# Performance work log

Measured on AMD Instinct MI355X. Metric: run time of the kernel, lower is better.

Reference implementation:

```python
import jax, jax.numpy as jnp
import numpy as np

B, T, D, H, L, O = 256, 256, 64, 512, 2, 10


def _uniform(key, shape, scale):
    return jax.random.uniform(key, shape, jnp.float32, -scale, scale)


def setup_inputs() -> dict:
    key = jax.random.key(0)
    ks = jax.random.split(key, 16)
    s = 1.0 / np.sqrt(H)  # PyTorch default init bound for RNN and Linear(H, .)
    inp = {
        "x": jax.random.normal(ks[0], (B, T, D), jnp.float32),
        # layer 0: input D -> H
        "w_ih0": _uniform(ks[1], (H, D), s),
        "w_hh0": _uniform(ks[2], (H, H), s),
        "b_ih0": _uniform(ks[3], (H,), s),
        "b_hh0": _uniform(ks[4], (H,), s),
        # layer 1: H -> H
        "w_ih1": _uniform(ks[5], (H, H), s),
        "w_hh1": _uniform(ks[6], (H, H), s),
        "b_ih1": _uniform(ks[7], (H,), s),
        "b_hh1": _uniform(ks[8], (H,), s),
        # head: fc1 (H->8), fc2 (8->O)
        "fc1_w": _uniform(ks[9], (8, H), s),
        "fc1_b": _uniform(ks[10], (8,), s),
        "fc2_w": _uniform(ks[11], (O, 8), 1.0 / np.sqrt(8)),
        "fc2_b": _uniform(ks[12], (O,), 1.0 / np.sqrt(8)),
    }
    return inp


def _rnn_relu_layer(seq, w_ih, w_hh, b_ih, b_hh):
    # seq: [T, B, Din] -> out: [T, B, H]
    # Precompute input projection for all timesteps (one big GEMM).
    x_proj = jnp.einsum('tbd,hd->tbh', seq, w_ih) + b_ih + b_hh

    def step(h, xp):
        h = jax.nn.relu(xp + h @ w_hh.T)
        return h, h

    h0 = jnp.zeros((seq.shape[1], w_hh.shape[0]), seq.dtype)
    _, out = jax.lax.scan(step, h0, x_proj)
    return out


def reference(x, w_ih0, w_hh0, b_ih0, b_hh0, w_ih1, w_hh1, b_ih1, b_hh1,
              fc1_w, fc1_b, fc2_w, fc2_b):
    seq = jnp.transpose(x, (1, 0, 2))  # [T, B, D]
    seq = _rnn_relu_layer(seq, w_ih0, w_hh0, b_ih0, b_hh0)
    seq = _rnn_relu_layer(seq, w_ih1, w_hh1, b_ih1, b_hh1)
    last = seq[-1]  # [B, H]
    h = jax.nn.relu(last @ fc1_w.T + fc1_b)
    return h @ fc2_w.T + fc2_b  # [B, O]
```

## Files before the change

### kernel.cpp

```cpp
#include <hip/hip_runtime.h>

using bf16x8 = __attribute__((ext_vector_type(8))) short;
using f32x4  = __attribute__((ext_vector_type(4))) float;
typedef unsigned short u16;
typedef unsigned int   u32;
typedef unsigned long long u64;

#define MAX_SPIN 1000000


__device__ __forceinline__ float bf2f(u16 u){ union{u32 i;float f;}v; v.i=((u32)u)<<16; return v.f; }
__device__ __forceinline__ u16 f2bf(float f){ union{float f;u32 i;}v; v.f=f; u32 x=v.i; return (u16)((x+0x7FFFu+((x>>16)&1u))>>16); }
__device__ __forceinline__ u32 packhl(float v){ u16 hi=f2bf(v); u16 lo=f2bf(v-bf2f(hi)); return ((u32)hi<<16)|(u32)lo; }
__device__ __forceinline__ bf16x8 load8f(const float* p){
  float4 a=*(const float4*)p; float4 b=*(const float4*)(p+4);
  bf16x8 r; r[0]=(short)f2bf(a.x); r[1]=(short)f2bf(a.y); r[2]=(short)f2bf(a.z); r[3]=(short)f2bf(a.w);
  r[4]=(short)f2bf(b.x); r[5]=(short)f2bf(b.y); r[6]=(short)f2bf(b.z); r[7]=(short)f2bf(b.w); return r;
}
__device__ __forceinline__ int  ldf(const int* p){ return __hip_atomic_load(p, __ATOMIC_RELAXED, __HIP_MEMORY_SCOPE_AGENT); }
__device__ __forceinline__ u64 ld64c(const u32* p){ return __hip_atomic_load((const u64*)p, __ATOMIC_RELAXED, __HIP_MEMORY_SCOPE_AGENT); }
__device__ __forceinline__ u32 ld32c(const u32* p){ return __hip_atomic_load(p, __ATOMIC_RELAXED, __HIP_MEMORY_SCOPE_AGENT); }
__device__ __forceinline__ void st32c(u32* p, u32 v){ __hip_atomic_store(p, v, __ATOMIC_RELAXED, __HIP_MEMORY_SCOPE_AGENT); }

__global__ void init_kernel(u32* p){
  p[(blockIdx.x<<9) + threadIdx.x] = 0u;
}

__global__ void __launch_bounds__(512, 2)
rnn_kernel(const float* __restrict__ x,
           const float* __restrict__ w_ih0, const float* __restrict__ w_hh0,
           const float* __restrict__ b_ih0, const float* __restrict__ b_hh0,
           const float* __restrict__ w_ih1, const float* __restrict__ w_hh1,
           const float* __restrict__ b_ih1, const float* __restrict__ b_hh1,
           const float* __restrict__ fc1_w, const float* __restrict__ fc1_b,
           const float* __restrict__ fc2_w, const float* __restrict__ fc2_b,
           float* __restrict__ out,
           u32* __restrict__ ring0, u32* __restrict__ ring1,
           int* __restrict__ fl0, int* __restrict__ fl1)
{
  const int tid  = threadIdx.x;
  const int wg   = blockIdx.x;
  const int lane = tid & 63;
  const int ww   = tid >> 6;
  const int role = wg >> 4;
  const int bt   = wg & 15;
  const int b0   = bt << 4;
  const int lrow = lane & 15;
  const int lk8  = (lane >> 4) << 3;
  const int sw   = (lrow & 7) << 4;

  __shared__ char smA[32768];
  __shared__ char smB[32768];

  if (role < 2) {
    const int nbase = role << 8;
    bf16x8 wH0[16], wH1[16], wX0[2], wX1[2];
    float bias0, bias1;
    {
      const int n0c = nbase + (ww << 5) + lrow;
      const int n1c = n0c + 16;
#pragma unroll
      for (int ks = 0; ks < 16; ++ks) {
        wH0[ks] = load8f(w_hh0 + n0c*512 + (ks<<5) + lk8);
        wH1[ks] = load8f(w_hh0 + n1c*512 + (ks<<5) + lk8);
      }
      wX0[0] = load8f(w_ih0 + n0c*64 + lk8);  wX0[1] = load8f(w_ih0 + n0c*64 + 32 + lk8);
      wX1[0] = load8f(w_ih0 + n1c*64 + lk8);  wX1[1] = load8f(w_ih0 + n1c*64 + 32 + lk8);
      bias0 = b_ih0[n0c] + b_hh0[n0c];
      bias1 = b_ih0[n1c] + b_hh0[n1c];
    }

    for (int s = 0; s < 256; ++s) {
      {
        int idx = tid << 1, r = idx >> 6, c = idx & 63;
        const float* xp = x + ((size_t)((b0 + r) << 8) + s) * 64 + c;
        float2 xv = *(const float2*)xp;
        u32 e0 = packhl(xv.x), e1 = packhl(xv.y);
        u32 hiw = (e0 >> 16) | (e1 & 0xFFFF0000u);
        u32 low = (e0 & 0xFFFFu) | (e1 << 16);
        int xo = (r << 7) + (((c << 1)) ^ ((r & 7) << 4));
        *(u32*)(smB + xo) = hiw;  *(u32*)(smB + 16384 + xo) = low;
      }
      __syncthreads();
      f32x4 acc0 = {0.f,0.f,0.f,0.f}, acc1 = {0.f,0.f,0.f,0.f};
#pragma unroll
      for (int ks = 0; ks < 2; ++ks) {
        int off = (lrow << 7) + (((ks << 6) + (lk8 << 1)) ^ sw);
        bf16x8 ahi = *(const bf16x8*)(smB + off);
        bf16x8 alo = *(const bf16x8*)(smB + 16384 + off);
        acc0 = __builtin_amdgcn_mfma_f32_16x16x32_bf16(ahi, wX0[ks], acc0, 0,0,0);
        acc0 = __builtin_amdgcn_mfma_f32_16x16x32_bf16(alo, wX0[ks], acc0, 0,0,0);
        acc1 = __builtin_amdgcn_mfma_f32_16x16x32_bf16(ahi, wX1[ks], acc1, 0,0,0);
        acc1 = __builtin_amdgcn_mfma_f32_16x16x32_bf16(alo, wX1[ks], acc1, 0,0,0);
      }
      if (ww == 0) {
        const int* f0p = fl0 + ((s - 1) << 4) + bt;
        const int* f1p = fl1 + ((s - 4) << 4) + bt;
        int it = 0;
        for (;;) {
          bool ok = true;
          if (s >= 1 && ldf(f0p) < 2) ok = false;
          if (ok && s >= 4 && ldf(f1p) < 4) ok = false;
          if (ok || ++it > MAX_SPIN) break;
        }
      }
      __syncthreads();
      if (s >= 1) {
        const u32* rs = ring0 + (((s - 1) & 3) << 17) + (b0 << 9);
#pragma unroll
        for (int k = 0; k < 8; ++k) {
          int q = tid + (k << 9);
          int r = q >> 8, c = q & 255;
          u64 v = ld64c(rs + (r << 9) + (c << 1));
          u32 e0 = (u32)v, e1 = (u32)(v >> 32);
          u32 hiw = (e0 >> 16) | (e1 & 0xFFFF0000u);
          u32 low = (e0 & 0xFFFFu) | (e1 << 16);
          int o = (r << 10) + ((c << 2) ^ ((r & 7) << 4));
          *(u32*)(smA + o) = hiw;  *(u32*)(smA + 16384 + o) = low;
        }
        __syncthreads();
#pragma unroll
        for (int ks = 0; ks < 16; ++ks) {
          int off = (lrow << 10) + (((ks << 6) + (lk8 << 1)) ^ sw);
          bf16x8 ahi = *(const bf16x8*)(smA + off);
          bf16x8 alo = *(const bf16x8*)(smA + 16384 + off);
          acc0 = __builtin_amdgcn_mfma_f32_16x16x32_bf16(ahi, wH0[ks], acc0, 0,0,0);
          acc0 = __builtin_amdgcn_mfma_f32_16x16x32_bf16(alo, wH0[ks], acc0, 0,0,0);
          acc1 = __builtin_amdgcn_mfma_f32_16x16x32_bf16(ahi, wH1[ks], acc1, 0,0,0);
          acc1 = __builtin_amdgcn_mfma_f32_16x16x32_bf16(alo, wH1[ks], acc1, 0,0,0);
        }
      }
      {
        u32* wsl = ring0 + ((s & 3) << 17) + (b0 << 9);
        int rr0 = (lane >> 4) << 2;
        int nc0 = nbase + (ww << 5) + lrow, nc1 = nc0 + 16;
#pragma unroll
        for (int r = 0; r < 4; ++r) {
          float v0 = acc0[r] + bias0; v0 = v0 > 0.f ? v0 : 0.f;
          float v1 = acc1[r] + bias1; v1 = v1 > 0.f ? v1 : 0.f;
          st32c(wsl + ((rr0 + r) << 9) + nc0, packhl(v0));
          st32c(wsl + ((rr0 + r) << 9) + nc1, packhl(v1));
        }
      }
      asm volatile("s_waitcnt vmcnt(0)" ::: "memory");
      __syncthreads();
      if (tid == 0)
        __hip_atomic_fetch_add(fl0 + (s << 4) + bt, 1, __ATOMIC_RELAXED, __HIP_MEMORY_SCOPE_AGENT);
    }
  } else {
    const int nbase = (role - 2) << 7;
    bf16x8 wI[16], wHH[16];
    float bias;
    {
      const int n = nbase + (ww << 4) + lrow;
#pragma unroll
      for (int ks = 0; ks < 16; ++ks) {
        wI[ks]  = load8f(w_ih1 + n*512 + (ks<<5) + lk8);
        wHH[ks] = load8f(w_hh1 + n*512 + (ks<<5) + lk8);
      }
      bias = b_ih1[n] + b_hh1[n];
    }

    for (int t = 0; t < 256; ++t) {
      if (ww == 0) {
        const int* f0p = fl0 + (t << 4) + bt;
        const int* f1p = fl1 + ((t - 1) << 4) + bt;
        int it = 0;
        for (;;) {
          bool ok = (ldf(f0p) >= 2);
          if (ok && t >= 1 && ldf(f1p) < 4) ok = false;
          if (ok || ++it > MAX_SPIN) break;
        }
      }
      __syncthreads();
      {
        const u32* ra = ring0 + ((t & 3) << 17) + (b0 << 9);
        const u32* rb = ring1 + (((t - 1) & 3) << 17) + (b0 << 9);
#pragma unroll
        for (int k = 0; k < 8; ++k) {
          int q = tid + (k << 9);
          int r = q >> 8, c = q & 255;
          int o = (r << 10) + ((c << 2) ^ ((r & 7) << 4));
          u64 v = ld64c(ra + (r << 9) + (c << 1));
          u32 e0 = (u32)v, e1 = (u32)(v >> 32);
          *(u32*)(smA + o)         = (e0 >> 16) | (e1 & 0xFFFF0000u);
          *(u32*)(smA + 16384 + o) = (e0 & 0xFFFFu) | (e1 << 16);
          if (t >= 1) {
            u64 w = ld64c(rb + (r << 9) + (c << 1));
            u32 f0v = (u32)w, f1v = (u32)(w >> 32);
            *(u32*)(smB + o)         = (f0v >> 16) | (f1v & 0xFFFF0000u);
            *(u32*)(smB + 16384 + o) = (f0v & 0xFFFFu) | (f1v << 16);
          }
        }
      }
      __syncthreads();
      f32x4 acc = {0.f,0.f,0.f,0.f};
      if (t == 0) {
#pragma unroll
        for (int ks = 0; ks < 16; ++ks) {
          int off = (lrow << 10) + (((ks << 6) + (lk8 << 1)) ^ sw);
          bf16x8 ahi = *(const bf16x8*)(smA + off);
          bf16x8 alo = *(const bf16x8*)(smA + 16384 + off);
          acc = __builtin_amdgcn_mfma_f32_16x16x32_bf16(ahi, wI[ks], acc, 0,0,0);
          acc = __builtin_amdgcn_mfma_f32_16x16x32_bf16(alo, wI[ks], acc, 0,0,0);
        }
      } else {
#pragma unroll
        for (int ks = 0; ks < 16; ++ks) {
          int off = (lrow << 10) + (((ks << 6) + (lk8 << 1)) ^ sw);
          bf16x8 ahi = *(const bf16x8*)(smA + off);
          bf16x8 alo = *(const bf16x8*)(smA + 16384 + off);
          bf16x8 bhi = *(const bf16x8*)(smB + off);
          bf16x8 blo = *(const bf16x8*)(smB + 16384 + off);
          acc = __builtin_amdgcn_mfma_f32_16x16x32_bf16(ahi, wI[ks],  acc, 0,0,0);
          acc = __builtin_amdgcn_mfma_f32_16x16x32_bf16(alo, wI[ks],  acc, 0,0,0);
          acc = __builtin_amdgcn_mfma_f32_16x16x32_bf16(bhi, wHH[ks], acc, 0,0,0);
          acc = __builtin_amdgcn_mfma_f32_16x16x32_bf16(blo, wHH[ks], acc, 0,0,0);
        }
      }
      {
        u32* wsl = ring1 + ((t & 3) << 17) + (b0 << 9);
        int rr0 = (lane >> 4) << 2;
        int nc = nbase + (ww << 4) + lrow;
#pragma unroll
        for (int r = 0; r < 4; ++r) {
          float v = acc[r] + bias; v = v > 0.f ? v : 0.f;
          st32c(wsl + ((rr0 + r) << 9) + nc, packhl(v));
        }
      }
      asm volatile("s_waitcnt vmcnt(0)" ::: "memory");
      __syncthreads();
      if (tid == 0)
        __hip_atomic_fetch_add(fl1 + (t << 4) + bt, 1, __ATOMIC_RELAXED, __HIP_MEMORY_SCOPE_AGENT);
    }

    if (role == 2) {
      if (ww == 0) {
        const int* fp = fl1 + (255 << 4) + bt;
        int it = 0;
        while (ldf(fp) < 4) { if (++it > MAX_SPIN) break; }
      }
      __syncthreads();
      float* smF = (float*)smA;
      if (tid < 128) {
        int b = b0 + (tid >> 3), j = tid & 7;
        const u32* hp = ring1 + (3 << 17) + (b << 9);
        const float* wr = fc1_w + (j << 9);
        float accv = fc1_b[j];
        for (int k = 0; k < 512; k += 2) {
          u64 v = ld64c(hp + k);
          u32 e0 = (u32)v, e1 = (u32)(v >> 32);
          float h0v = bf2f((u16)(e0 >> 16)) + bf2f((u16)(e0 & 0xFFFFu));
          float h1v = bf2f((u16)(e1 >> 16)) + bf2f((u16)(e1 & 0xFFFFu));
          accv += h0v * wr[k] + h1v * wr[k + 1];
        }
        smF[tid] = accv > 0.f ? accv : 0.f;
      }
      __syncthreads();
      if (tid < 160) {
        int bb = tid / 10, o = tid - bb * 10;
        float accv = fc2_b[o];
        const float* w = fc2_w + (o << 3);
#pragma unroll
        for (int j = 0; j < 8; ++j) accv += smF[(bb << 3) + j] * w[j];
        out[(b0 + bb) * 10 + o] = accv;
      }
    }
  }
}

extern "C" void kernel_launch(void* const* d_in, const int* in_sizes, int n_in,
                              void* d_out, int out_size, void* d_ws, size_t ws_size,
                              hipStream_t stream) {
  const float* x     = (const float*)d_in[0];
  const float* w_ih0 = (const float*)d_in[1];
  const float* w_hh0 = (const float*)d_in[2];
  const float* b_ih0 = (const float*)d_in[3];
  const float* b_hh0 = (const float*)d_in[4];
  const float* w_ih1 = (const float*)d_in[5];
  const float* w_hh1 = (const float*)d_in[6];
  const float* b_ih1 = (const float*)d_in[7];
  const float* b_hh1 = (const float*)d_in[8];
  const float* fc1_w = (const float*)d_in[9];
  const float* fc1_b = (const float*)d_in[10];
  const float* fc2_w = (const float*)d_in[11];
  const float* fc2_b = (const float*)d_in[12];
  float* out = (float*)d_out;

  char* ws = (char*)d_ws;
  u32* ring0 = (u32*)(ws);
  u32* ring1 = (u32*)(ws + (2 << 20));
  int* fl0   = (int*)(ws + (4 << 20));
  int* fl1   = (int*)(ws + (4 << 20) + 16384);

  init_kernel<<<dim3(16), dim3(512), 0, stream>>>((u32*)(ws + (4 << 20)));
  rnn_kernel<<<dim3(96), dim3(512), 0, stream>>>(
      x, w_ih0, w_hh0, b_ih0, b_hh0, w_ih1, w_hh1, b_ih1, b_hh1,
      fc1_w, fc1_b, fc2_w, fc2_b, out, ring0, ring1, fl0, fl1);
}
```

Measured before the change: 1.667 ms.

## Restructure RNN pipeline into per-batch-tile role workgroups with keeps-own-state recurrence

Reorganizes the persistent kernel into five roles per batch tile: a layer-0 recurrent WG and a layer-1 recurrent WG that each hold the full hidden state in LDS, two WGs computing the layer-1 input projection, and one WG computing the layer-0 input projection ahead of time. Each recurrent WG keeps W_hh partly in registers and partly in LDS, so the serial recurrence no longer needs a cross-workgroup exchange of the hidden state through global memory every step. Only precomputed projections go through global rings, with simple monotonic per-tile flags and s_sleep backoff. The cost is a large 160KB LDS footprint per WG and a longer dependency chain across more workgroups, which adds deadlock risk if not all 80 WGs are co-resident.

```diff
diff --git a/kernel.cpp b/kernel.cpp
--- a/kernel.cpp
+++ b/kernel.cpp
@@ -6,25 +6,30 @@
 typedef unsigned int   u32;
 typedef unsigned long long u64;
 
-#define MAX_SPIN 1000000
+#define MAX_SPIN 2000000
 
 
 __device__ __forceinline__ float bf2f(u16 u){ union{u32 i;float f;}v; v.i=((u32)u)<<16; return v.f; }
 __device__ __forceinline__ u16 f2bf(float f){ union{float f;u32 i;}v; v.f=f; u32 x=v.i; return (u16)((x+0x7FFFu+((x>>16)&1u))>>16); }
-__device__ __forceinline__ u32 packhl(float v){ u16 hi=f2bf(v); u16 lo=f2bf(v-bf2f(hi)); return ((u32)hi<<16)|(u32)lo; }
 __device__ __forceinline__ bf16x8 load8f(const float* p){
   float4 a=*(const float4*)p; float4 b=*(const float4*)(p+4);
   bf16x8 r; r[0]=(short)f2bf(a.x); r[1]=(short)f2bf(a.y); r[2]=(short)f2bf(a.z); r[3]=(short)f2bf(a.w);
   r[4]=(short)f2bf(b.x); r[5]=(short)f2bf(b.y); r[6]=(short)f2bf(b.z); r[7]=(short)f2bf(b.w); return r;
 }
-__device__ __forceinline__ int  ldf(const int* p){ return __hip_atomic_load(p, __ATOMIC_RELAXED, __HIP_MEMORY_SCOPE_AGENT); }
-__device__ __forceinline__ u64 ld64c(const u32* p){ return __hip_atomic_load((const u64*)p, __ATOMIC_RELAXED, __HIP_MEMORY_SCOPE_AGENT); }
-__device__ __forceinline__ u32 ld32c(const u32* p){ return __hip_atomic_load(p, __ATOMIC_RELAXED, __HIP_MEMORY_SCOPE_AGENT); }
+__device__ __forceinline__ int  ldf(int* p){ return __hip_atomic_load(p, __ATOMIC_RELAXED, __HIP_MEMORY_SCOPE_AGENT); }
+__device__ __forceinline__ void stf(int* p, int v){ __hip_atomic_store(p, v, __ATOMIC_RELAXED, __HIP_MEMORY_SCOPE_AGENT); }
+__device__ __forceinline__ u64  ld64c(const u32* p){ return __hip_atomic_load((const u64*)p, __ATOMIC_RELAXED, __HIP_MEMORY_SCOPE_AGENT); }
+__device__ __forceinline__ u32  ld32c(const u32* p){ return __hip_atomic_load(p, __ATOMIC_RELAXED, __HIP_MEMORY_SCOPE_AGENT); }
 __device__ __forceinline__ void st32c(u32* p, u32 v){ __hip_atomic_store(p, v, __ATOMIC_RELAXED, __HIP_MEMORY_SCOPE_AGENT); }
-
-__global__ void init_kernel(u32* p){
-  p[(blockIdx.x<<9) + threadIdx.x] = 0u;
+__device__ __forceinline__ int waitge(int* p, int tgt){
+  int v = ldf(p); int it = 0;
+  while (v < tgt && ++it < MAX_SPIN){ __builtin_amdgcn_s_sleep(1); v = ldf(p); }
+  return v;
 }
+
+__global__ void init_kernel(u32* p){ p[(blockIdx.x<<9) + threadIdx.x] = 0u; }
+
+#define HFRAG(base, ks) (*(const bf16x8*)((base) + (lrow<<10) + ((((ks)<<6)+(lk8<<1)) ^ sw)))
 
 __global__ void __launch_bounds__(512, 2)
 rnn_kernel(const float* __restrict__ x,
@@ -35,8 +40,8 @@
            const float* __restrict__ fc1_w, const float* __restrict__ fc1_b,
            const float* __restrict__ fc2_w, const float* __restrict__ fc2_b,
            float* __restrict__ out,
-           u32* __restrict__ ring0, u32* __restrict__ ring1,
-           int* __restrict__ fl0, int* __restrict__ fl1)
+           u32* __restrict__ ring0, u32* __restrict__ ringz0, u32* __restrict__ ringz1,
+           int* __restrict__ flags)
 {
   const int tid  = threadIdx.x;
   const int wg   = blockIdx.x;
@@ -48,223 +53,281 @@
   const int lrow = lane & 15;
   const int lk8  = (lane >> 4) << 3;
   const int sw   = (lrow & 7) << 4;
-
-  __shared__ char smA[32768];
-  __shared__ char smB[32768];
-
-  if (role < 2) {
-    const int nbase = role << 8;
-    bf16x8 wH0[16], wH1[16], wX0[2], wX1[2];
-    float bias0, bias1;
-    {
-      const int n0c = nbase + (ww << 5) + lrow;
-      const int n1c = n0c + 16;
-#pragma unroll
-      for (int ks = 0; ks < 16; ++ks) {
-        wH0[ks] = load8f(w_hh0 + n0c*512 + (ks<<5) + lk8);
-        wH1[ks] = load8f(w_hh0 + n1c*512 + (ks<<5) + lk8);
-      }
-      wX0[0] = load8f(w_ih0 + n0c*64 + lk8);  wX0[1] = load8f(w_ih0 + n0c*64 + 32 + lk8);
-      wX1[0] = load8f(w_ih0 + n1c*64 + lk8);  wX1[1] = load8f(w_ih0 + n1c*64 + 32 + lk8);
-      bias0 = b_ih0[n0c] + b_hh0[n0c];
-      bias1 = b_ih0[n1c] + b_hh0[n1c];
+  const int rb   = (lane >> 4) << 2;
+
+  extern __shared__ char dummy_unused[];
+  __shared__ char sm[163840];
+  char* smWb  = sm;
+  char* smHhi = sm + 131072;
+  char* smHlo = sm + 147456;
+
+  int* flA  = flags + ((bt<<3) + 0)*16;
+  int* flB0 = flags + ((bt<<3) + 1)*16;
+  int* flB1 = flags + ((bt<<3) + 2)*16;
+  int* flC  = flags + ((bt<<3) + 3)*16;
+  int* flD  = flags + ((bt<<3) + 4)*16;
+
+  if (role == 0 || role == 1) {
+    const float* Wp = (role == 0) ? w_hh0 : w_hh1;
+    const int n0 = ww << 6;
+    bf16x8 wv[48];
+#pragma unroll
+    for (int tt = 0; tt < 4; ++tt) {
+      int n = n0 + (tt<<4) + lrow;
+#pragma unroll
+      for (int ks = 0; ks < 12; ++ks)
+        wv[tt*12+ks] = load8f(Wp + n*512 + (ks<<5) + lk8);
+    }
+#pragma unroll 1
+    for (int it = 0; it < 16; ++it) {
+      int cid = (it<<9) + tid;
+      int ss = cid >> 11, wc = cid & 2047;
+      int n = wc >> 2, k0 = (wc & 3) << 3;
+      bf16x8 v = load8f(Wp + n*512 + 384 + (ss<<5) + k0);
+      *(bf16x8*)(smWb + (ss<<15) + (n<<6) + ((k0<<1) ^ ((n&3)<<4))) = v;
+    }
+    __syncthreads();
+
+    const int wl0 = ((lane>>4)<<4) ^ ((lrow&3)<<4);
+    int wlb[4];
+#pragma unroll
+    for (int tt = 0; tt < 4; ++tt) wlb[tt] = ((n0 + (tt<<4) + lrow)<<6) + wl0;
+
+    float zpf[16];
+    int f0v = 0, f1v = 0;
+    u32* zring = (role == 0) ? ringz0 : ringz1;
+    const u32* zbase = zring + bt*32768;
+    if (role == 0) { f0v = waitge(flD, 1); }
+    else           { f0v = waitge(flB0, 1); f1v = waitge(flB1, 1); }
+#pragma unroll
+    for (int tt = 0; tt < 4; ++tt) {
+      int nc = n0 + (tt<<4) + lrow;
+#pragma unroll
+      for (int r = 0; r < 4; ++r)
+        zpf[tt*4+r] = __uint_as_float(ld32c(zbase + ((rb+r)<<9) + nc));
     }
 
     for (int s = 0; s < 256; ++s) {
-      {
-        int idx = tid << 1, r = idx >> 6, c = idx & 63;
-        const float* xp = x + ((size_t)((b0 + r) << 8) + s) * 64 + c;
-        float2 xv = *(const float2*)xp;
-        u32 e0 = packhl(xv.x), e1 = packhl(xv.y);
-        u32 hiw = (e0 >> 16) | (e1 & 0xFFFF0000u);
-        u32 low = (e0 & 0xFFFFu) | (e1 << 16);
-        int xo = (r << 7) + (((c << 1)) ^ ((r & 7) << 4));
-        *(u32*)(smB + xo) = hiw;  *(u32*)(smB + 16384 + xo) = low;
-      }
-      __syncthreads();
-      f32x4 acc0 = {0.f,0.f,0.f,0.f}, acc1 = {0.f,0.f,0.f,0.f};
-#pragma unroll
-      for (int ks = 0; ks < 2; ++ks) {
-        int off = (lrow << 7) + (((ks << 6) + (lk8 << 1)) ^ sw);
-        bf16x8 ahi = *(const bf16x8*)(smB + off);
-        bf16x8 alo = *(const bf16x8*)(smB + 16384 + off);
-        acc0 = __builtin_amdgcn_mfma_f32_16x16x32_bf16(ahi, wX0[ks], acc0, 0,0,0);
-        acc0 = __builtin_amdgcn_mfma_f32_16x16x32_bf16(alo, wX0[ks], acc0, 0,0,0);
-        acc1 = __builtin_amdgcn_mfma_f32_16x16x32_bf16(ahi, wX1[ks], acc1, 0,0,0);
-        acc1 = __builtin_amdgcn_mfma_f32_16x16x32_bf16(alo, wX1[ks], acc1, 0,0,0);
-      }
-      if (ww == 0) {
-        const int* f0p = fl0 + ((s - 1) << 4) + bt;
-        const int* f1p = fl1 + ((s - 4) << 4) + bt;
-        int it = 0;
-        for (;;) {
-          bool ok = true;
-          if (s >= 1 && ldf(f0p) < 2) ok = false;
-          if (ok && s >= 4 && ldf(f1p) < 4) ok = false;
-          if (ok || ++it > MAX_SPIN) break;
-        }
-      }
-      __syncthreads();
-      if (s >= 1) {
-        const u32* rs = ring0 + (((s - 1) & 3) << 17) + (b0 << 9);
-#pragma unroll
-        for (int k = 0; k < 8; ++k) {
-          int q = tid + (k << 9);
-          int r = q >> 8, c = q & 255;
-          u64 v = ld64c(rs + (r << 9) + (c << 1));
-          u32 e0 = (u32)v, e1 = (u32)(v >> 32);
-          u32 hiw = (e0 >> 16) | (e1 & 0xFFFF0000u);
-          u32 low = (e0 & 0xFFFFu) | (e1 << 16);
-          int o = (r << 10) + ((c << 2) ^ ((r & 7) << 4));
-          *(u32*)(smA + o) = hiw;  *(u32*)(smA + 16384 + o) = low;
-        }
-        __syncthreads();
+      f32x4 acc[4] = {{0,0,0,0},{0,0,0,0},{0,0,0,0},{0,0,0,0}};
+      if (s > 0) {
 #pragma unroll
         for (int ks = 0; ks < 16; ++ks) {
-          int off = (lrow << 10) + (((ks << 6) + (lk8 << 1)) ^ sw);
-          bf16x8 ahi = *(const bf16x8*)(smA + off);
-          bf16x8 alo = *(const bf16x8*)(smA + 16384 + off);
-          acc0 = __builtin_amdgcn_mfma_f32_16x16x32_bf16(ahi, wH0[ks], acc0, 0,0,0);
-          acc0 = __builtin_amdgcn_mfma_f32_16x16x32_bf16(alo, wH0[ks], acc0, 0,0,0);
-          acc1 = __builtin_amdgcn_mfma_f32_16x16x32_bf16(ahi, wH1[ks], acc1, 0,0,0);
-          acc1 = __builtin_amdgcn_mfma_f32_16x16x32_bf16(alo, wH1[ks], acc1, 0,0,0);
-        }
-      }
-      {
-        u32* wsl = ring0 + ((s & 3) << 17) + (b0 << 9);
-        int rr0 = (lane >> 4) << 2;
-        int nc0 = nbase + (ww << 5) + lrow, nc1 = nc0 + 16;
+          bf16x8 ahi = HFRAG(smHhi, ks);
+          bf16x8 alo = HFRAG(smHlo, ks);
+          bf16x8 bw0, bw1, bw2, bw3;
+          if (ks < 12) { bw0 = wv[ks]; bw1 = wv[12+ks]; bw2 = wv[24+ks]; bw3 = wv[36+ks]; }
+          else {
+            int sb = (ks-12) << 15;
+            bw0 = *(const bf16x8*)(smWb + sb + wlb[0]);
+            bw1 = *(const bf16x8*)(smWb + sb + wlb[1]);
+            bw2 = *(const bf16x8*)(smWb + sb + wlb[2]);
+            bw3 = *(const bf16x8*)(smWb + sb + wlb[3]);
+          }
+          acc[0] = __builtin_amdgcn_mfma_f32_16x16x32_bf16(ahi, bw0, acc[0], 0,0,0);
+          acc[0] = __builtin_amdgcn_mfma_f32_16x16x32_bf16(alo, bw0, acc[0], 0,0,0);
+          acc[1] = __builtin_amdgcn_mfma_f32_16x16x32_bf16(ahi, bw1, acc[1], 0,0,0);
+          acc[1] = __builtin_amdgcn_mfma_f32_16x16x32_bf16(alo, bw1, acc[1], 0,0,0);
+          acc[2] = __builtin_amdgcn_mfma_f32_16x16x32_bf16(ahi, bw2, acc[2], 0,0,0);
+          acc[2] = __builtin_amdgcn_mfma_f32_16x16x32_bf16(alo, bw2, acc[2], 0,0,0);
+          acc[3] = __builtin_amdgcn_mfma_f32_16x16x32_bf16(ahi, bw3, acc[3], 0,0,0);
+          acc[3] = __builtin_amdgcn_mfma_f32_16x16x32_bf16(alo, bw3, acc[3], 0,0,0);
+        }
+      }
+      u32 pk[16];
+#pragma unroll
+      for (int tt = 0; tt < 4; ++tt)
 #pragma unroll
         for (int r = 0; r < 4; ++r) {
-          float v0 = acc0[r] + bias0; v0 = v0 > 0.f ? v0 : 0.f;
-          float v1 = acc1[r] + bias1; v1 = v1 > 0.f ? v1 : 0.f;
-          st32c(wsl + ((rr0 + r) << 9) + nc0, packhl(v0));
-          st32c(wsl + ((rr0 + r) << 9) + nc1, packhl(v1));
-        }
-      }
-      asm volatile("s_waitcnt vmcnt(0)" ::: "memory");
-      __syncthreads();
-      if (tid == 0)
-        __hip_atomic_fetch_add(fl0 + (s << 4) + bt, 1, __ATOMIC_RELAXED, __HIP_MEMORY_SCOPE_AGENT);
-    }
-  } else {
-    const int nbase = (role - 2) << 7;
-    bf16x8 wI[16], wHH[16];
-    float bias;
-    {
-      const int n = nbase + (ww << 4) + lrow;
-#pragma unroll
-      for (int ks = 0; ks < 16; ++ks) {
-        wI[ks]  = load8f(w_ih1 + n*512 + (ks<<5) + lk8);
-        wHH[ks] = load8f(w_hh1 + n*512 + (ks<<5) + lk8);
-      }
-      bias = b_ih1[n] + b_hh1[n];
-    }
-
-    for (int t = 0; t < 256; ++t) {
-      if (ww == 0) {
-        const int* f0p = fl0 + (t << 4) + bt;
-        const int* f1p = fl1 + ((t - 1) << 4) + bt;
-        int it = 0;
-        for (;;) {
-          bool ok = (ldf(f0p) >= 2);
-          if (ok && t >= 1 && ldf(f1p) < 4) ok = false;
-          if (ok || ++it > MAX_SPIN) break;
-        }
-      }
-      __syncthreads();
-      {
-        const u32* ra = ring0 + ((t & 3) << 17) + (b0 << 9);
-        const u32* rb = ring1 + (((t - 1) & 3) << 17) + (b0 << 9);
-#pragma unroll
-        for (int k = 0; k < 8; ++k) {
-          int q = tid + (k << 9);
-          int r = q >> 8, c = q & 255;
-          int o = (r << 10) + ((c << 2) ^ ((r & 7) << 4));
-          u64 v = ld64c(ra + (r << 9) + (c << 1));
-          u32 e0 = (u32)v, e1 = (u32)(v >> 32);
-          *(u32*)(smA + o)         = (e0 >> 16) | (e1 & 0xFFFF0000u);
-          *(u32*)(smA + 16384 + o) = (e0 & 0xFFFFu) | (e1 << 16);
-          if (t >= 1) {
-            u64 w = ld64c(rb + (r << 9) + (c << 1));
-            u32 f0v = (u32)w, f1v = (u32)(w >> 32);
-            *(u32*)(smB + o)         = (f0v >> 16) | (f1v & 0xFFFF0000u);
-            *(u32*)(smB + 16384 + o) = (f0v & 0xFFFFu) | (f1v << 16);
+          float v = acc[tt][r] + zpf[tt*4+r];
+          v = v > 0.f ? v : 0.f;
+          u16 hi = f2bf(v); u16 lo = f2bf(v - bf2f(hi));
+          pk[tt*4+r] = ((u32)hi << 16) | lo;
+        }
+      if (role == 0) {
+        u32* rs = ring0 + bt*32768 + ((s&3)<<13);
+#pragma unroll
+        for (int tt = 0; tt < 4; ++tt) {
+          int nc = n0 + (tt<<4) + lrow;
+#pragma unroll
+          for (int r = 0; r < 4; ++r) st32c(rs + ((rb+r)<<9) + nc, pk[tt*4+r]);
+        }
+      }
+      __syncthreads();
+#pragma unroll
+      for (int tt = 0; tt < 4; ++tt) {
+        int cc = n0 + (tt<<4) + lrow;
+#pragma unroll
+        for (int r = 0; r < 4; ++r) {
+          int rr = rb + r;
+          int o = (rr<<10) + (((cc<<1)) ^ ((rr&7)<<4));
+          *(u16*)(smHhi + o) = (u16)(pk[tt*4+r] >> 16);
+          *(u16*)(smHlo + o) = (u16)(pk[tt*4+r] & 0xFFFFu);
+        }
+      }
+      if (role == 0) asm volatile("s_waitcnt vmcnt(0)" ::: "memory");
+      __syncthreads();
+      if (tid == 0) stf((role==0) ? flA : flC, s + 1);
+      if (s < 255) {
+        if (role == 0) {
+          if (f0v < s+2) f0v = waitge(flD, s+2); else f0v = ldf(flD);
+          int need = s - 2;
+          if (need > 0) {
+            int bv0 = ldf(flB0), bv1 = ldf(flB1);
+            if (bv0 < need) waitge(flB0, need);
+            if (bv1 < need) waitge(flB1, need);
           }
-        }
-      }
-      __syncthreads();
-      f32x4 acc = {0.f,0.f,0.f,0.f};
-      if (t == 0) {
-#pragma unroll
-        for (int ks = 0; ks < 16; ++ks) {
-          int off = (lrow << 10) + (((ks << 6) + (lk8 << 1)) ^ sw);
-          bf16x8 ahi = *(const bf16x8*)(smA + off);
-          bf16x8 alo = *(const bf16x8*)(smA + 16384 + off);
-          acc = __builtin_amdgcn_mfma_f32_16x16x32_bf16(ahi, wI[ks], acc, 0,0,0);
-          acc = __builtin_amdgcn_mfma_f32_16x16x32_bf16(alo, wI[ks], acc, 0,0,0);
-        }
-      } else {
-#pragma unroll
-        for (int ks = 0; ks < 16; ++ks) {
-          int off = (lrow << 10) + (((ks << 6) + (lk8 << 1)) ^ sw);
-          bf16x8 ahi = *(const bf16x8*)(smA + off);
-          bf16x8 alo = *(const bf16x8*)(smA + 16384 + off);
-          bf16x8 bhi = *(const bf16x8*)(smB + off);
-          bf16x8 blo = *(const bf16x8*)(smB + 16384 + off);
-          acc = __builtin_amdgcn_mfma_f32_16x16x32_bf16(ahi, wI[ks],  acc, 0,0,0);
-          acc = __builtin_amdgcn_mfma_f32_16x16x32_bf16(alo, wI[ks],  acc, 0,0,0);
-          acc = __builtin_amdgcn_mfma_f32_16x16x32_bf16(bhi, wHH[ks], acc, 0,0,0);
-          acc = __builtin_amdgcn_mfma_f32_16x16x32_bf16(blo, wHH[ks], acc, 0,0,0);
-        }
-      }
-      {
-        u32* wsl = ring1 + ((t & 3) << 17) + (b0 << 9);
-        int rr0 = (lane >> 4) << 2;
-        int nc = nbase + (ww << 4) + lrow;
-#pragma unroll
-        for (int r = 0; r < 4; ++r) {
-          float v = acc[r] + bias; v = v > 0.f ? v : 0.f;
-          st32c(wsl + ((rr0 + r) << 9) + nc, packhl(v));
-        }
-      }
-      asm volatile("s_waitcnt vmcnt(0)" ::: "memory");
-      __syncthreads();
-      if (tid == 0)
-        __hip_atomic_fetch_add(fl1 + (t << 4) + bt, 1, __ATOMIC_RELAXED, __HIP_MEMORY_SCOPE_AGENT);
-    }
-
-    if (role == 2) {
-      if (ww == 0) {
-        const int* fp = fl1 + (255 << 4) + bt;
-        int it = 0;
-        while (ldf(fp) < 4) { if (++it > MAX_SPIN) break; }
-      }
-      __syncthreads();
-      float* smF = (float*)smA;
+        } else {
+          if (f0v < s+2) f0v = waitge(flB0, s+2); else f0v = ldf(flB0);
+          if (f1v < s+2) f1v = waitge(flB1, s+2); else f1v = ldf(flB1);
+        }
+        const u32* zs = zbase + (((s+1)&3)<<13);
+#pragma unroll
+        for (int tt = 0; tt < 4; ++tt) {
+          int nc = n0 + (tt<<4) + lrow;
+#pragma unroll
+          for (int r = 0; r < 4; ++r)
+            zpf[tt*4+r] = __uint_as_float(ld32c(zs + ((rb+r)<<9) + nc));
+        }
+      }
+    }
+
+    if (role == 1) {
+      float* smF = (float*)sm;
       if (tid < 128) {
-        int b = b0 + (tid >> 3), j = tid & 7;
-        const u32* hp = ring1 + (3 << 17) + (b << 9);
+        int r = tid >> 3, j = tid & 7;
         const float* wr = fc1_w + (j << 9);
         float accv = fc1_b[j];
-        for (int k = 0; k < 512; k += 2) {
-          u64 v = ld64c(hp + k);
-          u32 e0 = (u32)v, e1 = (u32)(v >> 32);
-          float h0v = bf2f((u16)(e0 >> 16)) + bf2f((u16)(e0 & 0xFFFFu));
-          float h1v = bf2f((u16)(e1 >> 16)) + bf2f((u16)(e1 & 0xFFFFu));
-          accv += h0v * wr[k] + h1v * wr[k + 1];
+        for (int k = 0; k < 512; ++k) {
+          int o = (r<<10) + (((k<<1)) ^ ((r&7)<<4));
+          float hv = bf2f(*(u16*)(smHhi + o)) + bf2f(*(u16*)(smHlo + o));
+          accv += hv * wr[k];
         }
         smF[tid] = accv > 0.f ? accv : 0.f;
       }
       __syncthreads();
       if (tid < 160) {
-        int bb = tid / 10, o = tid - bb * 10;
+        int bb = tid / 10, o = tid - bb*10;
         float accv = fc2_b[o];
         const float* w = fc2_w + (o << 3);
 #pragma unroll
-        for (int j = 0; j < 8; ++j) accv += smF[(bb << 3) + j] * w[j];
-        out[(b0 + bb) * 10 + o] = accv;
-      }
+        for (int j = 0; j < 8; ++j) accv += smF[(bb<<3)+j] * w[j];
+        out[(b0 + bb)*10 + o] = accv;
+      }
+    }
+  } else if (role == 2 || role == 3) {
+    const int nb = (role - 2) << 8;
+    const int n0 = nb + (ww << 5);
+    bf16x8 wv[32];
+    float bias[2];
+#pragma unroll
+    for (int tt = 0; tt < 2; ++tt) {
+      int n = n0 + (tt<<4) + lrow;
+#pragma unroll
+      for (int ks = 0; ks < 16; ++ks)
+        wv[tt*16+ks] = load8f(w_ih1 + n*512 + (ks<<5) + lk8);
+      bias[tt] = b_ih1[n] + b_hh1[n];
+    }
+    int* flB = (role == 2) ? flB0 : flB1;
+    int flAv = waitge(flA, 1), flCv = 0;
+    u64 pf[8];
+    {
+      const u32* rs = ring0 + bt*32768;
+#pragma unroll
+      for (int k = 0; k < 8; ++k) {
+        int q = tid + (k<<9); int r = q >> 8, c = q & 255;
+        pf[k] = ld64c(rs + (r<<9) + (c<<1));
+      }
+    }
+    for (int t = 0; t < 256; ++t) {
+#pragma unroll
+      for (int k = 0; k < 8; ++k) {
+        int q = tid + (k<<9); int r = q >> 8, c = q & 255;
+        u32 e0 = (u32)pf[k], e1 = (u32)(pf[k] >> 32);
+        int o = (r<<10) + ((c<<2) ^ ((r&7)<<4));
+        *(u32*)(smHhi + o) = (e0 >> 16) | (e1 & 0xFFFF0000u);
+        *(u32*)(smHlo + o) = (e0 & 0xFFFFu) | (e1 << 16);
+      }
+      __syncthreads();
+      f32x4 acc[2] = {{0,0,0,0},{0,0,0,0}};
+#pragma unroll
+      for (int ks = 0; ks < 16; ++ks) {
+        bf16x8 ahi = HFRAG(smHhi, ks);
+        bf16x8 alo = HFRAG(smHlo, ks);
+        acc[0] = __builtin_amdgcn_mfma_f32_16x16x32_bf16(ahi, wv[ks],    acc[0], 0,0,0);
+        acc[0] = __builtin_amdgcn_mfma_f32_16x16x32_bf16(alo, wv[ks],    acc[0], 0,0,0);
+        acc[1] = __builtin_amdgcn_mfma_f32_16x16x32_bf16(ahi, wv[16+ks], acc[1], 0,0,0);
+        acc[1] = __builtin_amdgcn_mfma_f32_16x16x32_bf16(alo, wv[16+ks], acc[1], 0,0,0);
+      }
+      {
+        u32* zs = ringz1 + bt*32768 + ((t&3)<<13);
+#pragma unroll
+        for (int tt = 0; tt < 2; ++tt) {
+          int nc = n0 + (tt<<4) + lrow;
+#pragma unroll
+          for (int r = 0; r < 4; ++r)
+            st32c(zs + ((rb+r)<<9) + nc, __float_as_uint(acc[tt][r] + bias[tt]));
+        }
+      }
+      __syncthreads();
+      asm volatile("s_waitcnt vmcnt(0)" ::: "memory");
+      __syncthreads();
+      if (tid == 0) stf(flB, t + 1);
+      if (t < 255) {
+        if (flAv < t+2) flAv = waitge(flA, t+2); else flAv = ldf(flA);
+        int need = t - 2;
+        if (need > 0 && flCv < need) flCv = waitge(flC, need);
+        else flCv = ldf(flC);
+        const u32* rs = ring0 + bt*32768 + (((t+1)&3)<<13);
+#pragma unroll
+        for (int k = 0; k < 8; ++k) {
+          int q = tid + (k<<9); int r = q >> 8, c = q & 255;
+          pf[k] = ld64c(rs + (r<<9) + (c<<1));
+        }
+      }
+    }
+  } else {
+    const int n0 = ww << 6;
+    bf16x8 wx[8];
+    float bz[4];
+#pragma unroll
+    for (int tt = 0; tt < 4; ++tt) {
+      int n = n0 + (tt<<4) + lrow;
+      wx[tt*2+0] = load8f(w_ih0 + n*64 + lk8);
+      wx[tt*2+1] = load8f(w_ih0 + n*64 + 32 + lk8);
+      bz[tt] = b_ih0[n] + b_hh0[n];
+    }
+    int flAv = 0;
+    for (int s = 0; s < 256; ++s) {
+      if (s >= 4 && flAv < s-3) flAv = waitge(flA, s-3);
+      bf16x8 xh0, xl0, xh1, xl1;
+      const float* xp = x + ((size_t)(b0 + lrow)*256 + s)*64 + lk8;
+#pragma unroll
+      for (int j = 0; j < 8; ++j) {
+        float f0 = xp[j], f1 = xp[32+j];
+        u16 h0 = f2bf(f0); xh0[j] = (short)h0; xl0[j] = (short)f2bf(f0 - bf2f(h0));
+        u16 h1 = f2bf(f1); xh1[j] = (short)h1; xl1[j] = (short)f2bf(f1 - bf2f(h1));
+      }
+      f32x4 acc[4] = {{0,0,0,0},{0,0,0,0},{0,0,0,0},{0,0,0,0}};
+#pragma unroll
+      for (int tt = 0; tt < 4; ++tt) {
+        acc[tt] = __builtin_amdgcn_mfma_f32_16x16x32_bf16(xh0, wx[tt*2+0], acc[tt], 0,0,0);
+        acc[tt] = __builtin_amdgcn_mfma_f32_16x16x32_bf16(xl0, wx[tt*2+0], acc[tt], 0,0,0);
+        acc[tt] = __builtin_amdgcn_mfma_f32_16x16x32_bf16(xh1, wx[tt*2+1], acc[tt], 0,0,0);
+        acc[tt] = __builtin_amdgcn_mfma_f32_16x16x32_bf16(xl1, wx[tt*2+1], acc[tt], 0,0,0);
+      }
+      {
+        u32* zs = ringz0 + bt*32768 + ((s&3)<<13);
+#pragma unroll
+        for (int tt = 0; tt < 4; ++tt) {
+          int nc = n0 + (tt<<4) + lrow;
+#pragma unroll
+          for (int r = 0; r < 4; ++r)
+            st32c(zs + ((rb+r)<<9) + nc, __float_as_uint(acc[tt][r] + bz[tt]));
+        }
+      }
+      asm volatile("s_waitcnt vmcnt(0)" ::: "memory");
+      __syncthreads();
+      if (tid == 0) stf(flD, s + 1);
     }
   }
 }
@@ -288,13 +351,14 @@
   float* out = (float*)d_out;
 
   char* ws = (char*)d_ws;
-  u32* ring0 = (u32*)(ws);
-  u32* ring1 = (u32*)(ws + (2 << 20));
-  int* fl0   = (int*)(ws + (4 << 20));
-  int* fl1   = (int*)(ws + (4 << 20) + 16384);
-
-  init_kernel<<<dim3(16), dim3(512), 0, stream>>>((u32*)(ws + (4 << 20)));
-  rnn_kernel<<<dim3(96), dim3(512), 0, stream>>>(
+  u32* ring0  = (u32*)(ws);
+  u32* ringz0 = (u32*)(ws + (2u<<20));
+  u32* ringz1 = (u32*)(ws + (4u<<20));
+  int* flags  = (int*)(ws + (6u<<20));
+
+  init_kernel<<<dim3(4), dim3(512), 0, stream>>>((u32*)(ws + (6u<<20)));
+  rnn_kernel<<<dim3(80), dim3(512), 0, stream>>>(
       x, w_ih0, w_hh0, b_ih0, b_hh0, w_ih1, w_hh1, b_ih1, b_hh1,
-      fc1_w, fc1_b, fc2_w, fc2_b, out, ring0, ring1, fl0, fl1);
+      fc1_w, fc1_b, fc2_w, fc2_b, out,
+      ring0, ringz0, ringz1, flags);
 }
```

New measurement: 2.059 ms. 1.24x slower.
